# Performance work log

Hardware: AMD Instinct MI355X
Metric: run time of the kernel (lower is better)

Reference implementation:

```python
import jax, jax.numpy as jnp
import numpy as np


def _l2norm(x, eps=1e-12):
    # F.normalize(p=2, dim=-1): x / max(||x||_2, eps)
    n = jnp.linalg.norm(x, axis=-1, keepdims=True)
    return x / jnp.maximum(n, eps)


def _dwconv3x3(x, w):
    # depthwise 3x3 conv, padding=1, no bias. x: [B,C,H,W], w: [C,1,3,3]
    return jax.lax.conv_general_dilated(
        x, w, window_strides=(1, 1), padding='SAME',
        feature_group_count=x.shape[1],
        dimension_numbers=('NCHW', 'OIHW', 'NCHW'))


def setup_inputs() -> dict:
    key = jax.random.key(0)
    ks = jax.random.split(key, 10)
    B, H, W, C = 2, 256, 256, 64
    heads, dh, dim_out = 8, 64, 64
    hd = heads * dh  # 512
    s = 0.02
    return {
        'x_in': jax.random.normal(ks[0], (B, H, W, C), jnp.float32),
        'Wq': jax.random.normal(ks[1], (C, hd), jnp.float32) * s,
        'Wk': jax.random.normal(ks[2], (C, hd), jnp.float32) * s,
        'Wv': jax.random.normal(ks[3], (C, hd), jnp.float32) * s,
        'rescale': jnp.ones((heads, 1, 1), jnp.float32),
        'Wproj': jax.random.normal(ks[4], (hd, dim_out), jnp.float32) * s,
        'bproj': jnp.zeros((dim_out,), jnp.float32),
        'Wc1d': jax.random.normal(ks[5], (hd, dim_out), jnp.float32) * s,
        'bc1d': jnp.zeros((dim_out,), jnp.float32),
        'Wpe1': jax.random.normal(ks[6], (dim_out, 1, 3, 3), jnp.float32) * s,
        'Wpe2': jax.random.normal(ks[7], (dim_out, 1, 3, 3), jnp.float32) * s,
    }


def reference(x_in, Wq, Wk, Wv, rescale, Wproj, bproj, Wc1d, bc1d, Wpe1, Wpe2):
    b, h, w, c = x_in.shape
    heads = rescale.shape[0]
    hd = Wq.shape[1]
    dh = hd // heads
    dim_out = Wproj.shape[1]
    ds = 2

    # AvgPool2d(2,2) on channels-last input
    xp = x_in.reshape(b, h // ds, ds, w // ds, ds, c).mean(axis=(2, 4))
    n_ds = (h // ds) * (w // ds)
    xd = xp.reshape(b, n_ds, c)

    # q,k from downsampled tokens; v from full-res tokens
    q = (xd @ Wq).reshape(b, n_ds, heads, dh).transpose(0, 2, 3, 1)   # [b,heads,dh,n_ds]
    k = (xd @ Wk).reshape(b, n_ds, heads, dh).transpose(0, 2, 3, 1)   # [b,heads,dh,n_ds]
    v_inp = x_in.reshape(b, h * w, c) @ Wv                             # [b,n,hd]
    v = v_inp.reshape(b, h * w, heads, dh).transpose(0, 2, 3, 1)       # [b,heads,dh,n]

    q = _l2norm(q)
    k = _l2norm(k)

    # channel (transposed) attention: [b,heads,dh,dh]
    attn = jnp.einsum('bhin,bhjn->bhij', k, q) * rescale
    attn = jax.nn.softmax(attn, axis=-1)

    xa = jnp.einsum('bhij,bhjn->bhin', attn, v)                        # [b,heads,dh,n]
    xa = xa.transpose(0, 3, 1, 2).reshape(b, h * w, hd)                # [b,n,hd]
    out_c = (xa @ Wproj + bproj).reshape(b, h, w, dim_out)

    # positional branch: 1x1 conv (pointwise) then two depthwise 3x3 convs with GELU
    p = v_inp @ Wc1d + bc1d                                            # [b,n,dim_out]
    p = p.reshape(b, h, w, dim_out).transpose(0, 3, 1, 2)              # [b,dim_out,h,w]
    p = _dwconv3x3(p, Wpe1)
    p = jax.nn.gelu(p, approximate=False)
    p = _dwconv3x3(p, Wpe2)
    out_p = p.transpose(0, 2, 3, 1)                                    # [b,h,w,dim_out]

    return out_c + out_p
```

## Files before the change

kernel.cpp:

```cpp
#include <hip/hip_runtime.h>
#include <math.h>


typedef unsigned short u16;
typedef unsigned int u32;
typedef __attribute__((ext_vector_type(8))) short short8;
typedef __attribute__((ext_vector_type(4))) float f32x4;

__device__ __forceinline__ float bf2f(u16 h) { return __uint_as_float(((u32)h) << 16); }
__device__ __forceinline__ u16 f2bf(float f) {
    u32 u = __float_as_uint(f);
    return (u16)((u + 0x7fffu + ((u >> 16) & 1u)) >> 16);
}
__device__ __forceinline__ float rbf(float f) { return bf2f(f2bf(f)); }
__device__ __forceinline__ u32 pk2(float lo, float hi) {
    return (u32)f2bf(lo) | ((u32)f2bf(hi) << 16);
}
__device__ __forceinline__ void unpack8(uint4 v, float* f) {
    u32 a[4] = {v.x, v.y, v.z, v.w};
#pragma unroll
    for (int i = 0; i < 4; ++i) {
        f[2 * i]     = __uint_as_float(a[i] << 16);
        f[2 * i + 1] = __uint_as_float(a[i] & 0xffff0000u);
    }
}
__device__ __forceinline__ float gelu_exact(float v) {
    return 0.5f * v * (1.f + erff(v * 0.70710678118654752f));
}
__device__ __forceinline__ void splitbf(float g, short& hi, short& lo) {
    u16 hb = f2bf(g);
    hi = (short)hb;
    lo = (short)f2bf(g - bf2f(hb));
}

__global__ __launch_bounds__(256) void k_front(
    const float* __restrict__ x,
    const float* __restrict__ wq_f, const float* __restrict__ wk_f,
    const float* __restrict__ wv_f, const float* __restrict__ rs_f,
    const float* __restrict__ wp_f, const float* __restrict__ bp_f,
    const float* __restrict__ wc_f, const float* __restrict__ bc_f,
    const float* __restrict__ p1_f, const float* __restrict__ p2_f,
    u32* __restrict__ wb32, u16* __restrict__ wqT, u16* __restrict__ wkT,
    u16* __restrict__ wpT, float* __restrict__ Wpos,
    u16* __restrict__ xb, float* __restrict__ partials) {
    __shared__ float xvs[64 * 68];
    int blk = blockIdx.x;
    int t = threadIdx.x;
    if (blk < 323) {
        u32 pid = (u32)blk * 256u + t;
        if (pid < 82564u) {
            const float* src; u32 p;
            if      (pid < 16384u) { src = wq_f; p = pid; }
            else if (pid < 32768u) { src = wk_f; p = pid - 16384u; }
            else if (pid < 49152u) { src = wv_f; p = pid - 32768u; }
            else if (pid < 49156u) { src = rs_f; p = pid - 49152u; }
            else if (pid < 65540u) { src = wp_f; p = pid - 49156u; }
            else if (pid < 65572u) { src = bp_f; p = pid - 65540u; }
            else if (pid < 81956u) { src = wc_f; p = pid - 65572u; }
            else if (pid < 81988u) { src = bc_f; p = pid - 81956u; }
            else if (pid < 82276u) { src = p1_f; p = pid - 81988u; }
            else                   { src = p2_f; p = pid - 82276u; }
            wb32[pid] = (u32)f2bf(src[2 * p]) | ((u32)f2bf(src[2 * p + 1]) << 16);
            if (pid < 32768u) {
                u16* dstT = (pid < 16384u) ? wqT : wkT;
                u32 e0 = 2u * (pid & 16383u);
                u32 c = e0 >> 9, j = e0 & 511u;
                dstT[j * 64 + c]       = f2bf(src[e0]);
                dstT[(j + 1) * 64 + c] = f2bf(src[e0 + 1]);
            } else if (pid >= 49156u && pid < 65540u) {
                u32 e0 = 2u * (pid - 49156u);
                u32 ip = e0 >> 6, o = e0 & 63u;
                u32 base = (ip >> 6) * 4096u + (ip & 63u);
                wpT[base + o * 64]       = f2bf(src[e0]);
                wpT[base + (o + 1) * 64] = f2bf(src[e0 + 1]);
            }
        }
    } else if (blk < 387) {
        int c = blk - 323;
        int o = t & 63, ch = t >> 6;
        const float* wvr = wv_f + c * 512 + ch * 128;
        const float* wcr = wc_f + (size_t)(ch * 128) * 64 + o;
        float s = 0.f;
        for (int kk = 0; kk < 128; ++kk)
            s += rbf(wvr[kk]) * rbf(wcr[(size_t)kk * 64]);
        xvs[ch * 64 + o] = s;
        __syncthreads();
        if (t < 64)
            Wpos[c * 64 + t] = (xvs[t] + xvs[64 + t]) + (xvs[128 + t] + xvs[192 + t]);
    } else {
        int gb = blk - 387;
        int b = gb >> 8, sub = gb & 255;
        int py = sub >> 1, half = sub & 1;
        const size_t rowbase = (size_t)(b * 256 + 2 * py) * 16384 + (size_t)half * 8192;
#pragma unroll
        for (int i2 = 0; i2 < 4; ++i2) {
            int u = t + 256 * i2;
            int P = u >> 4, cq = u & 15;
            size_t o0 = rowbase + (size_t)(2 * P) * 64 + cq * 4;
            float4 a0 = *(const float4*)(x + o0);
            float4 a1 = *(const float4*)(x + o0 + 64);
            float4 a2 = *(const float4*)(x + o0 + 16384);
            float4 a3 = *(const float4*)(x + o0 + 16384 + 64);
            *(uint2*)(xb + o0)              = make_uint2(pk2(a0.x, a0.y), pk2(a0.z, a0.w));
            *(uint2*)(xb + o0 + 64)         = make_uint2(pk2(a1.x, a1.y), pk2(a1.z, a1.w));
            *(uint2*)(xb + o0 + 16384)      = make_uint2(pk2(a2.x, a2.y), pk2(a2.z, a2.w));
            *(uint2*)(xb + o0 + 16384 + 64) = make_uint2(pk2(a3.x, a3.y), pk2(a3.z, a3.w));
            float4 s;
            s.x = 0.25f * (a0.x + a1.x + a2.x + a3.x);
            s.y = 0.25f * (a0.y + a1.y + a2.y + a3.y);
            s.z = 0.25f * (a0.z + a1.z + a2.z + a3.z);
            s.w = 0.25f * (a0.w + a1.w + a2.w + a3.w);
            *(float4*)(&xvs[P * 68 + cq * 4]) = s;
        }
        __syncthreads();
        int r0 = (t >> 4) << 2, c0 = (t & 15) << 2;
        float acc[4][4] = {{0.f}};
        for (int P = 0; P < 64; ++P) {
            float4 av = *(const float4*)(&xvs[P * 68 + r0]);
            float4 bv = *(const float4*)(&xvs[P * 68 + c0]);
            float ar[4] = {av.x, av.y, av.z, av.w};
            float br[4] = {bv.x, bv.y, bv.z, bv.w};
#pragma unroll
            for (int i = 0; i < 4; ++i)
#pragma unroll
                for (int j = 0; j < 4; ++j)
                    acc[i][j] += ar[i] * br[j];
        }
        float* outp = partials + (size_t)gb * 4096;
#pragma unroll
        for (int i = 0; i < 4; ++i)
            *(float4*)(&outp[(r0 + i) * 64 + c0]) =
                make_float4(acc[i][0], acc[i][1], acc[i][2], acc[i][3]);
    }
}

__global__ __launch_bounds__(256) void k_mid1(
    const float* __restrict__ partials, float* __restrict__ G4, float* __restrict__ Weff,
    const u16* __restrict__ xb, const float* __restrict__ Wpos,
    const u16* __restrict__ bc1d, u16* __restrict__ pbuf) {
    __shared__ u16 sm[128 * 72];
    int blk = blockIdx.x;
    int t = threadIdx.x;
    if (blk < 128) {
        int gid = blk * 256 + t;
        int e = gid & 4095, ch = (gid >> 12) & 3, b = gid >> 14;
        const float* p0 = partials + ((size_t)(b * 256 + ch * 64)) * 4096 + e;
        float s = 0.f;
        for (int p = 0; p < 64; ++p)
            s += p0[(size_t)p * 4096];
        G4[gid] = s;
        if (gid < 8192) Weff[gid] = 0.f;
        return;
    }
    int pb = blk - 128;
    int lane = t & 63, wv = t >> 6;
    int col = lane & 15, quad = lane >> 4;

    short8 bf[2][4];
#pragma unroll
    for (int kh = 0; kh < 2; ++kh)
#pragma unroll
        for (int nt = 0; nt < 4; ++nt) {
            short8 v;
#pragma unroll
            for (int j = 0; j < 8; ++j)
                v[j] = (short)f2bf(Wpos[(kh * 32 + quad * 8 + j) * 64 + nt * 16 + col]);
            bf[kh][nt] = v;
        }
    float bias[4];
#pragma unroll
    for (int nt = 0; nt < 4; ++nt) bias[nt] = bf2f(bc1d[nt * 16 + col]);

    size_t base = (size_t)pb * 128;
#pragma unroll
    for (int g = 0; g < 2; ++g) {
        int P0 = wv * 32 + g * 16;
        const short8* ap = (const short8*)(xb + (base + P0 + col) * 64);
        short8 a0 = ap[quad];
        short8 a1 = ap[4 + quad];
#pragma unroll
        for (int nt = 0; nt < 4; ++nt) {
            f32x4 acc = {0.f, 0.f, 0.f, 0.f};
            acc = __builtin_amdgcn_mfma_f32_16x16x32_bf16(a0, bf[0][nt], acc, 0, 0, 0);
            acc = __builtin_amdgcn_mfma_f32_16x16x32_bf16(a1, bf[1][nt], acc, 0, 0, 0);
#pragma unroll
            for (int r = 0; r < 4; ++r)
                sm[(P0 + quad * 4 + r) * 72 + nt * 16 + col] = f2bf(acc[r] + bias[nt]);
        }
    }
    __syncthreads();
#pragma unroll
    for (int k = 0; k < 4; ++k) {
        int linear = k * 256 + t;
        int px = linear >> 3, oct = linear & 7;
        uint4 v = *(const uint4*)(&sm[px * 72 + oct * 8]);
        *(uint4*)(pbuf + (base + px) * 64 + oct * 8) = v;
    }
}

__global__ __launch_bounds__(256) void k_mid2(
    const u16* __restrict__ wqT, const u16* __restrict__ wkT,
    const u16* __restrict__ wpT, const u16* __restrict__ wvb,
    const u16* __restrict__ rsb,
    const float* __restrict__ G4, float* __restrict__ Weff,
    const u16* __restrict__ pbuf, const u16* __restrict__ wpe1, u16* __restrict__ tbuf) {
    __shared__ __align__(16) char shm[53248];
    int blk = blockIdx.x, t = threadIdx.x;
    if (blk < 16) {
        u16*   GhiL = (u16*)shm;
        u16*   GloL = (u16*)(shm + 9216);
        float* Lraw = (float*)shm;
        float* TkS  = (float*)(shm + 18432);
        float* TqS  = (float*)(shm + 35840);
        int b = blk >> 3, h = blk & 7;
        int lane = t & 63, w = t >> 6;
        int lr = lane & 15, lq = lane >> 4;
        {
            int base = t * 16;
            int row = base >> 6, col = base & 63;
            const float* Gb = G4 + (size_t)b * 16384;
#pragma unroll
            for (int half = 0; half < 2; ++half) {
                short8 hi8, lo8;
#pragma unroll
                for (int q = 0; q < 8; ++q) {
                    int e = base + half * 8 + q;
                    float g = (Gb[e] + Gb[4096 + e]) + (Gb[8192 + e] + Gb[12288 + e]);
                    short hh, ll; splitbf(g, hh, ll);
                    hi8[q] = hh; lo8[q] = ll;
                }
                *(short8*)(&GhiL[row * 72 + col + half * 8]) = hi8;
                *(short8*)(&GloL[row * 72 + col + half * 8]) = lo8;
            }
        }
        __syncthreads();
        {
            short8 ahi[2], alo[2];
#pragma unroll
            for (int ks = 0; ks < 2; ++ks) {
                ahi[ks] = *(const short8*)(&GhiL[(w * 16 + lr) * 72 + ks * 32 + lq * 8]);
                alo[ks] = *(const short8*)(&GloL[(w * 16 + lr) * 72 + ks * 32 + lq * 8]);
            }
#pragma unroll
            for (int sel = 0; sel < 2; ++sel) {
                const u16* WT = sel ? wqT : wkT;
                float* outp = sel ? TqS : TkS;
#pragma unroll
                for (int nt = 0; nt < 4; ++nt) {
                    f32x4 acc = {0.f, 0.f, 0.f, 0.f};
#pragma unroll
                    for (int ks = 0; ks < 2; ++ks) {
                        short8 bv = *(const short8*)(&WT[(h * 64 + nt * 16 + lr) * 64 + ks * 32 + lq * 8]);
                        acc = __builtin_amdgcn_mfma_f32_16x16x32_bf16(ahi[ks], bv, acc, 0, 0, 0);
                        acc = __builtin_amdgcn_mfma_f32_16x16x32_bf16(alo[ks], bv, acc, 0, 0, 0);
                    }
#pragma unroll
                    for (int r = 0; r < 4; ++r)
                        outp[(w * 16 + lq * 4 + r) * 68 + nt * 16 + lr] = acc[r];
                }
            }
        }
        __syncthreads();
        {
            int ci = t & 63, grp = t >> 6;
            const u16* wr = wkT + (h * 64 + ci) * 64 + grp * 16;
            float s = 0.f;
#pragma unroll
            for (int cc = 0; cc < 16; ++cc)
                s += bf2f(wr[cc]) * TkS[(grp * 16 + cc) * 68 + ci];
            TqS[ci * 68 + 64 + grp] = s;
        }
        __syncthreads();
        if (t < 64) {
            float s = (TqS[t * 68 + 64] + TqS[t * 68 + 65]) +
                      (TqS[t * 68 + 66] + TqS[t * 68 + 67]);
            TkS[t * 68 + 64] = fmaxf(sqrtf(fmaxf(s, 0.f)), 1e-12f);
        }
        {
            short8 ak[2];
#pragma unroll
            for (int ks = 0; ks < 2; ++ks)
                ak[ks] = *(const short8*)(&wkT[(h * 64 + w * 16 + lr) * 64 + ks * 32 + lq * 8]);
#pragma unroll
            for (int nt = 0; nt < 4; ++nt) {
                f32x4 acc = {0.f, 0.f, 0.f, 0.f};
#pragma unroll
                for (int ks = 0; ks < 2; ++ks) {
                    short8 bhi, blo;
#pragma unroll
                    for (int jj = 0; jj < 8; ++jj) {
                        short h16, l16;
                        splitbf(TqS[(ks * 32 + lq * 8 + jj) * 68 + nt * 16 + lr], h16, l16);
                        bhi[jj] = h16; blo[jj] = l16;
                    }
                    acc = __builtin_amdgcn_mfma_f32_16x16x32_bf16(ak[ks], bhi, acc, 0, 0, 0);
                    acc = __builtin_amdgcn_mfma_f32_16x16x32_bf16(ak[ks], blo, acc, 0, 0, 0);
                }
#pragma unroll
                for (int r = 0; r < 4; ++r)
                    Lraw[(w * 16 + lq * 4 + r) * 68 + nt * 16 + lr] = acc[r];
            }
        }
        __syncthreads();
        {
            int ci = t & 63, grp = t >> 6;
            const u16* wr = wqT + (h * 64 + ci) * 64 + grp * 16;
            float s = 0.f;
#pragma unroll
            for (int cc = 0; cc < 16; ++cc)
                s += bf2f(wr[cc]) * TqS[(grp * 16 + cc) * 68 + ci];
            TqS[ci * 68 + 64 + grp] = s;
        }
        __syncthreads();
        if (t < 64) {
            float s = (TqS[t * 68 + 64] + TqS[t * 68 + 65]) +
                      (TqS[t * 68 + 66] + TqS[t * 68 + 67]);
            TkS[t * 68 + 65] = fmaxf(sqrtf(fmaxf(s, 0.f)), 1e-12f);
        }
        __syncthreads();
        {
            int i = t >> 2, jq = t & 3, j0 = jq * 16;
            float L[16];
#pragma unroll
            for (int q = 0; q < 4; ++q) {
                float4 lv = *(const float4*)(&Lraw[i * 68 + j0 + 4 * q]);
                L[4 * q] = lv.x; L[4 * q + 1] = lv.y;
                L[4 * q + 2] = lv.z; L[4 * q + 3] = lv.w;
            }
            float rs = bf2f(rsb[h]);
            float nki = TkS[i * 68 + 64];
            float nqv[16];
#pragma unroll
            for (int jj = 0; jj < 16; ++jj) nqv[jj] = TkS[(j0 + jj) * 68 + 65];
            float m = -1e30f;
#pragma unroll
            for (int jj = 0; jj < 16; ++jj) {
                L[jj] = L[jj] * rs / (nki * nqv[jj]);
                m = fmaxf(m, L[jj]);
            }
            m = fmaxf(m, __shfl_xor(m, 1));
            m = fmaxf(m, __shfl_xor(m, 2));
            float s = 0.f;
#pragma unroll
            for (int jj = 0; jj < 16; ++jj) {
                L[jj] = __expf(L[jj] - m);
                s += L[jj];
            }
            s += __shfl_xor(s, 1);
            s += __shfl_xor(s, 2);
            float inv = 1.f / s;
#pragma unroll
            for (int q = 0; q < 4; ++q)
                *(float4*)(&Lraw[i * 68 + j0 + 4 * q]) =
                    make_float4(L[4 * q] * inv, L[4 * q + 1] * inv,
                                L[4 * q + 2] * inv, L[4 * q + 3] * inv);
        }
        __syncthreads();
        {
            short8 ahi[2], alo[2];
#pragma unroll
            for (int ks = 0; ks < 2; ++ks) {
                short8 hi, lo;
#pragma unroll
                for (int jj = 0; jj < 8; ++jj) {
                    short h16, l16;
                    splitbf(Lraw[(ks * 32 + lq * 8 + jj) * 68 + w * 16 + lr], h16, l16);
                    hi[jj] = h16; lo[jj] = l16;
                }
                ahi[ks] = hi; alo[ks] = lo;
            }
#pragma unroll
            for (int nt = 0; nt < 4; ++nt) {
                f32x4 acc = {0.f, 0.f, 0.f, 0.f};
#pragma unroll
                for (int ks = 0; ks < 2; ++ks) {
                    short8 bv = *(const short8*)(&wpT[h * 4096 + (nt * 16 + lr) * 64 + ks * 32 + lq * 8]);
                    acc = __builtin_amdgcn_mfma_f32_16x16x32_bf16(ahi[ks], bv, acc, 0, 0, 0);
                    acc = __builtin_amdgcn_mfma_f32_16x16x32_bf16(alo[ks], bv, acc, 0, 0, 0);
                }
#pragma unroll
                for (int r = 0; r < 4; ++r)
                    TkS[(w * 16 + lq * 4 + r) * 68 + nt * 16 + lr] = acc[r];
            }
        }
        __syncthreads();
        {
            short8 av[2];
#pragma unroll
            for (int ks = 0; ks < 2; ++ks)
                av[ks] = *(const short8*)(&wvb[(w * 16 + lr) * 512 + h * 64 + ks * 32 + lq * 8]);
            float* W = Weff + b * 4096;
#pragma unroll
            for (int nt = 0; nt < 4; ++nt) {
                f32x4 acc = {0.f, 0.f, 0.f, 0.f};
#pragma unroll
                for (int ks = 0; ks < 2; ++ks) {
                    short8 bhi, blo;
#pragma unroll
                    for (int jj = 0; jj < 8; ++jj) {
                        short h16, l16;
                        splitbf(TkS[(ks * 32 + lq * 8 + jj) * 68 + nt * 16 + lr], h16, l16);
                        bhi[jj] = h16; blo[jj] = l16;
                    }
                    acc = __builtin_amdgcn_mfma_f32_16x16x32_bf16(av[ks], bhi, acc, 0, 0, 0);
                    acc = __builtin_amdgcn_mfma_f32_16x16x32_bf16(av[ks], blo, acc, 0, 0, 0);
                }
#pragma unroll
                for (int r = 0; r < 4; ++r)
                    atomicAdd(&W[(w * 16 + lq * 4 + r) * 64 + nt * 16 + lr], acc[r]);
            }
        }
        return;
    }
    u16* sm = (u16*)shm;
    int cb = blk - 16;
    int b  = cb >> 9;
    int ty = (cb >> 3) & 63;
    int tx = cb & 7;
    int gy0 = ty * 4, gx0 = tx * 32;

    for (int i = t; i < 1632; i += 256) {
        int px = i >> 3, ch = i & 7;
        int hy = px / 34, hx = px - hy * 34;
        int gy = gy0 + hy - 1, gx = gx0 + hx - 1;
        uint4 v = make_uint4(0, 0, 0, 0);
        if ((unsigned)gy < 256u && (unsigned)gx < 256u)
            v = *(const uint4*)(pbuf + ((size_t)((b << 16) + (gy << 8) + gx)) * 64 + ch * 8);
        *(uint4*)(&sm[px * 72 + ch * 8]) = v;
    }
    int oct = t & 7;
    float w[8][9];
#pragma unroll
    for (int j = 0; j < 8; ++j)
#pragma unroll
        for (int k = 0; k < 9; ++k) w[j][k] = bf2f(wpe1[(oct * 8 + j) * 9 + k]);
    __syncthreads();

#pragma unroll
    for (int s = 0; s < 4; ++s) {
        int lp = (t >> 3) + s * 32;
        int ly = lp >> 5, lx = lp & 31;
        float acc[8] = {0.f, 0.f, 0.f, 0.f, 0.f, 0.f, 0.f, 0.f};
#pragma unroll
        for (int dy = 0; dy < 3; ++dy)
#pragma unroll
            for (int dx = 0; dx < 3; ++dx) {
                int hp = (ly + dy) * 34 + lx + dx;
                uint4 v = *(const uint4*)(&sm[hp * 72 + oct * 8]);
                float f[8];
                unpack8(v, f);
                int tap = dy * 3 + dx;
#pragma unroll
                for (int j = 0; j < 8; ++j) acc[j] += f[j] * w[j][tap];
            }
        u32 pk[4];
#pragma unroll
        for (int q = 0; q < 4; ++q)
            pk[q] = pk2(gelu_exact(acc[2 * q]), gelu_exact(acc[2 * q + 1]));
        size_t gpix = (size_t)(b << 16) + ((size_t)(gy0 + ly) << 8) + gx0 + lx;
        *(uint4*)(tbuf + gpix * 64 + oct * 8) = make_uint4(pk[0], pk[1], pk[2], pk[3]);
    }
}

__global__ __launch_bounds__(256) void k_final(const u16* __restrict__ xb,
                                               const u16* __restrict__ tbuf,
                                               const float* __restrict__ Weff,
                                               const u16* __restrict__ wpe2,
                                               const u16* __restrict__ bproj,
                                               float* __restrict__ out) {
    __shared__ u16 sm[204 * 72];
    __shared__ float stage[128 * 68];
    int t = threadIdx.x;
    int blk = blockIdx.x;
    int b  = blk >> 9;
    int ty = (blk >> 3) & 63;
    int tx = blk & 7;
    int gy0 = ty * 4, gx0 = tx * 32;

    for (int i = t; i < 1632; i += 256) {
        int px = i >> 3, ch = i & 7;
        int hy = px / 34, hx = px - hy * 34;
        int gy = gy0 + hy - 1, gx = gx0 + hx - 1;
        uint4 v = make_uint4(0, 0, 0, 0);
        if ((unsigned)gy < 256u && (unsigned)gx < 256u)
            v = *(const uint4*)(tbuf + ((size_t)((b << 16) + (gy << 8) + gx)) * 64 + ch * 8);
        *(uint4*)(&sm[px * 72 + ch * 8]) = v;
    }
    int oct = t & 7;
    {
        float w[8][9];
#pragma unroll
        for (int j = 0; j < 8; ++j)
#pragma unroll
            for (int k = 0; k < 9; ++k) w[j][k] = bf2f(wpe2[(oct * 8 + j) * 9 + k]);
        __syncthreads();
#pragma unroll
        for (int s = 0; s < 4; ++s) {
            int lp = (t >> 3) + s * 32;
            int ly = lp >> 5, lx = lp & 31;
            float acc[8] = {0.f, 0.f, 0.f, 0.f, 0.f, 0.f, 0.f, 0.f};
#pragma unroll
            for (int dy = 0; dy < 3; ++dy)
#pragma unroll
                for (int dx = 0; dx < 3; ++dx) {
                    int hp = (ly + dy) * 34 + lx + dx;
                    uint4 v = *(const uint4*)(&sm[hp * 72 + oct * 8]);
                    float f[8];
                    unpack8(v, f);
                    int tap = dy * 3 + dx;
#pragma unroll
                    for (int j = 0; j < 8; ++j) acc[j] += f[j] * w[j][tap];
                }
#pragma unroll
            for (int j = 0; j < 8; ++j)
                stage[lp * 68 + oct * 8 + j] = acc[j];
        }
    }
    __syncthreads();

    int lane = t & 63, wv = t >> 6;
    int col = lane & 15, quad = lane >> 4;
    const float* W = Weff + b * 4096;
    short8 bf[2][4];
#pragma unroll
    for (int kh = 0; kh < 2; ++kh)
#pragma unroll
        for (int nt = 0; nt < 4; ++nt) {
            short8 v;
#pragma unroll
            for (int j = 0; j < 8; ++j)
                v[j] = (short)f2bf(W[(kh * 32 + quad * 8 + j) * 64 + nt * 16 + col]);
            bf[kh][nt] = v;
        }
    float bias[4];
#pragma unroll
    for (int nt = 0; nt < 4; ++nt) bias[nt] = bf2f(bproj[nt * 16 + col]);

#pragma unroll
    for (int g = 0; g < 2; ++g) {
        int grp = wv * 2 + g;
        int ly = grp >> 1;
        int lxb = (grp & 1) * 16;
        size_t rowpix = (size_t)(b << 16) + ((size_t)(gy0 + ly) << 8) + gx0;
        const short8* ap = (const short8*)(xb + (rowpix + lxb + col) * 64);
        short8 a0 = ap[quad];
        short8 a1 = ap[4 + quad];
#pragma unroll
        for (int nt = 0; nt < 4; ++nt) {
            f32x4 acc = {0.f, 0.f, 0.f, 0.f};
            acc = __builtin_amdgcn_mfma_f32_16x16x32_bf16(a0, bf[0][nt], acc, 0, 0, 0);
            acc = __builtin_amdgcn_mfma_f32_16x16x32_bf16(a1, bf[1][nt], acc, 0, 0, 0);
#pragma unroll
            for (int r = 0; r < 4; ++r) {
                int lp = ly * 32 + lxb + quad * 4 + r;
                stage[lp * 68 + nt * 16 + col] += acc[r] + bias[nt];
            }
        }
    }
    __syncthreads();

#pragma unroll
    for (int k = 0; k < 8; ++k) {
        int linear = k * 256 + t;
        int px = linear >> 4, c4 = linear & 15;
        int ly = px >> 5, lx = px & 31;
        float4 v = *(const float4*)(&stage[px * 68 + c4 * 4]);
        size_t gpix = (size_t)(b << 16) + ((size_t)(gy0 + ly) << 8) + gx0 + lx;
        *(float4*)(out + gpix * 64 + c4 * 4) = v;
    }
}

extern "C" void kernel_launch(void* const* d_in, const int* in_sizes, int n_in,
                              void* d_out, int out_size, void* d_ws, size_t ws_size,
                              hipStream_t stream) {
    const float* x = (const float*)d_in[0];
    float* out = (float*)d_out;

    char* w = (char*)d_ws;
    size_t off = 0;
    auto alloc = [&](size_t bytes) -> void* {
        void* p = w + off;
        off += (bytes + 255) & ~(size_t)255;
        return p;
    };
    u16* xb = (u16*)alloc((size_t)16777216 * 2);
    u16* wb = (u16*)alloc((size_t)165128 * 2);
    u16* wqb = wb;
    u16* wkb = wqb + 32768;
    u16* wvb = wkb + 32768;
    u16* rsb = wvb + 32768;
    u16* wpb = rsb + 8;
    u16* bpb = wpb + 32768;
    u16* wcb = bpb + 64;
    u16* bcb = wcb + 32768;
    u16* p1b = bcb + 64;
    u16* p2b = p1b + 576;
    (void)wcb; (void)wqb; (void)wkb; (void)wpb;

    u16* wqT = (u16*)alloc((size_t)32768 * 2);
    u16* wkT = (u16*)alloc((size_t)32768 * 2);
    u16* wpT = (u16*)alloc((size_t)32768 * 2);

    float* partials = (float*)alloc((size_t)512 * 4096 * 4);
    float* G4       = (float*)alloc((size_t)2 * 4 * 4096 * 4);
    float* Weff     = (float*)alloc((size_t)2 * 4096 * 4);
    float* Wpos     = (float*)alloc((size_t)4096 * 4);
    u16*   pbuf     = (u16*)alloc((size_t)2 * 65536 * 64 * 2);
    u16*   tbuf     = (u16*)alloc((size_t)2 * 65536 * 64 * 2);

    hipLaunchKernelGGL(k_front, dim3(899), dim3(256), 0, stream,
                       x,
                       (const float*)d_in[1], (const float*)d_in[2], (const float*)d_in[3],
                       (const float*)d_in[4], (const float*)d_in[5], (const float*)d_in[6],
                       (const float*)d_in[7], (const float*)d_in[8], (const float*)d_in[9],
                       (const float*)d_in[10],
                       (u32*)wb, wqT, wkT, wpT, Wpos, xb, partials);
    hipLaunchKernelGGL(k_mid1, dim3(1152), dim3(256), 0, stream,
                       partials, G4, Weff, xb, Wpos, bcb, pbuf);
    hipLaunchKernelGGL(k_mid2, dim3(1040), dim3(256), 0, stream,
                       wqT, wkT, wpT, wvb, rsb, G4, Weff, pbuf, p1b, tbuf);
    hipLaunchKernelGGL(k_final, dim3(1024), dim3(256), 0, stream,
                       xb, tbuf, Weff, p2b, bpb, out);
}
```

Before: 155.1 us.

## Fuse Gram reduction via atomics and recompute pointwise conv inside dwconv tiles

```diff
diff --git a/kernel.cpp b/kernel.cpp
--- a/kernel.cpp
+++ b/kernel.cpp
@@ -42,7 +42,7 @@
     const float* __restrict__ p1_f, const float* __restrict__ p2_f,
     u32* __restrict__ wb32, u16* __restrict__ wqT, u16* __restrict__ wkT,
     u16* __restrict__ wpT, float* __restrict__ Wpos,
-    u16* __restrict__ xb, float* __restrict__ partials) {
+    u16* __restrict__ xb, float* __restrict__ G4) {
     __shared__ float xvs[64 * 68];
     int blk = blockIdx.x;
     int t = threadIdx.x;
@@ -126,75 +126,12 @@
                 for (int j = 0; j < 4; ++j)
                     acc[i][j] += ar[i] * br[j];
         }
-        float* outp = partials + (size_t)gb * 4096;
+        float* gout = G4 + ((size_t)(b * 4 + (sub & 3))) * 4096;
 #pragma unroll
         for (int i = 0; i < 4; ++i)
-            *(float4*)(&outp[(r0 + i) * 64 + c0]) =
-                make_float4(acc[i][0], acc[i][1], acc[i][2], acc[i][3]);
-    }
-}
-
-__global__ __launch_bounds__(256) void k_mid1(
-    const float* __restrict__ partials, float* __restrict__ G4, float* __restrict__ Weff,
-    const u16* __restrict__ xb, const float* __restrict__ Wpos,
-    const u16* __restrict__ bc1d, u16* __restrict__ pbuf) {
-    __shared__ u16 sm[128 * 72];
-    int blk = blockIdx.x;
-    int t = threadIdx.x;
-    if (blk < 128) {
-        int gid = blk * 256 + t;
-        int e = gid & 4095, ch = (gid >> 12) & 3, b = gid >> 14;
-        const float* p0 = partials + ((size_t)(b * 256 + ch * 64)) * 4096 + e;
-        float s = 0.f;
-        for (int p = 0; p < 64; ++p)
-            s += p0[(size_t)p * 4096];
-        G4[gid] = s;
-        if (gid < 8192) Weff[gid] = 0.f;
-        return;
-    }
-    int pb = blk - 128;
-    int lane = t & 63, wv = t >> 6;
-    int col = lane & 15, quad = lane >> 4;
-
-    short8 bf[2][4];
-#pragma unroll
-    for (int kh = 0; kh < 2; ++kh)
-#pragma unroll
-        for (int nt = 0; nt < 4; ++nt) {
-            short8 v;
-#pragma unroll
-            for (int j = 0; j < 8; ++j)
-                v[j] = (short)f2bf(Wpos[(kh * 32 + quad * 8 + j) * 64 + nt * 16 + col]);
-            bf[kh][nt] = v;
-        }
-    float bias[4];
-#pragma unroll
-    for (int nt = 0; nt < 4; ++nt) bias[nt] = bf2f(bc1d[nt * 16 + col]);
-
-    size_t base = (size_t)pb * 128;
-#pragma unroll
-    for (int g = 0; g < 2; ++g) {
-        int P0 = wv * 32 + g * 16;
-        const short8* ap = (const short8*)(xb + (base + P0 + col) * 64);
-        short8 a0 = ap[quad];
-        short8 a1 = ap[4 + quad];
-#pragma unroll
-        for (int nt = 0; nt < 4; ++nt) {
-            f32x4 acc = {0.f, 0.f, 0.f, 0.f};
-            acc = __builtin_amdgcn_mfma_f32_16x16x32_bf16(a0, bf[0][nt], acc, 0, 0, 0);
-            acc = __builtin_amdgcn_mfma_f32_16x16x32_bf16(a1, bf[1][nt], acc, 0, 0, 0);
-#pragma unroll
-            for (int r = 0; r < 4; ++r)
-                sm[(P0 + quad * 4 + r) * 72 + nt * 16 + col] = f2bf(acc[r] + bias[nt]);
-        }
-    }
-    __syncthreads();
-#pragma unroll
-    for (int k = 0; k < 4; ++k) {
-        int linear = k * 256 + t;
-        int px = linear >> 3, oct = linear & 7;
-        uint4 v = *(const uint4*)(&sm[px * 72 + oct * 8]);
-        *(uint4*)(pbuf + (base + px) * 64 + oct * 8) = v;
+#pragma unroll
+            for (int j = 0; j < 4; ++j)
+                atomicAdd(&gout[(r0 + i) * 64 + c0 + j], acc[i][j]);
     }
 }
 
@@ -203,7 +140,9 @@
     const u16* __restrict__ wpT, const u16* __restrict__ wvb,
     const u16* __restrict__ rsb,
     const float* __restrict__ G4, float* __restrict__ Weff,
-    const u16* __restrict__ pbuf, const u16* __restrict__ wpe1, u16* __restrict__ tbuf) {
+    const u16* __restrict__ xb, const float* __restrict__ Wpos,
+    const u16* __restrict__ bc1d, const u16* __restrict__ wpe1,
+    u16* __restrict__ tbuf) {
     __shared__ __align__(16) char shm[53248];
     int blk = blockIdx.x, t = threadIdx.x;
     if (blk < 16) {
@@ -418,15 +357,56 @@
     int ty = (cb >> 3) & 63;
     int tx = cb & 7;
     int gy0 = ty * 4, gx0 = tx * 32;
-
-    for (int i = t; i < 1632; i += 256) {
-        int px = i >> 3, ch = i & 7;
-        int hy = px / 34, hx = px - hy * 34;
-        int gy = gy0 + hy - 1, gx = gx0 + hx - 1;
-        uint4 v = make_uint4(0, 0, 0, 0);
-        if ((unsigned)gy < 256u && (unsigned)gx < 256u)
-            v = *(const uint4*)(pbuf + ((size_t)((b << 16) + (gy << 8) + gx)) * 64 + ch * 8);
-        *(uint4*)(&sm[px * 72 + ch * 8]) = v;
+    {
+        int lane = t & 63, wv = t >> 6;
+        int col = lane & 15, quad = lane >> 4;
+        short8 bfw[2][4];
+#pragma unroll
+        for (int kh = 0; kh < 2; ++kh)
+#pragma unroll
+            for (int nt = 0; nt < 4; ++nt) {
+                short8 v;
+#pragma unroll
+                for (int j = 0; j < 8; ++j)
+                    v[j] = (short)f2bf(Wpos[(kh * 32 + quad * 8 + j) * 64 + nt * 16 + col]);
+                bfw[kh][nt] = v;
+            }
+        float bias[4];
+#pragma unroll
+        for (int nt = 0; nt < 4; ++nt) bias[nt] = bf2f(bc1d[nt * 16 + col]);
+#pragma unroll
+        for (int g = 0; g < 4; ++g) {
+            int grp = wv * 4 + g;
+            int pa = grp * 16 + col;
+            int hya = pa / 34, hxa = pa - hya * 34;
+            int gya = gy0 + hya - 1, gxa = gx0 + hxa - 1;
+            bool ina = ((unsigned)gya < 256u) && ((unsigned)gxa < 256u) && (pa < 204);
+            size_t pix = ina ? ((size_t)(b << 16) + ((size_t)gya << 8) + gxa) : 0;
+            const short8* ap = (const short8*)(xb + pix * 64);
+            short8 a0 = ap[quad];
+            short8 a1 = ap[4 + quad];
+            f32x4 accs[4];
+#pragma unroll
+            for (int nt = 0; nt < 4; ++nt) {
+                f32x4 acc = {0.f, 0.f, 0.f, 0.f};
+                acc = __builtin_amdgcn_mfma_f32_16x16x32_bf16(a0, bfw[0][nt], acc, 0, 0, 0);
+                acc = __builtin_amdgcn_mfma_f32_16x16x32_bf16(a1, bfw[1][nt], acc, 0, 0, 0);
+                accs[nt] = acc;
+            }
+#pragma unroll
+            for (int r = 0; r < 4; ++r) {
+                int pc = grp * 16 + quad * 4 + r;
+                if (pc < 204) {
+                    int hyc = pc / 34, hxc = pc - hyc * 34;
+                    int gyc = gy0 + hyc - 1, gxc = gx0 + hxc - 1;
+                    bool inc = ((unsigned)gyc < 256u) && ((unsigned)gxc < 256u);
+#pragma unroll
+                    for (int nt = 0; nt < 4; ++nt)
+                        sm[pc * 72 + nt * 16 + col] =
+                            inc ? f2bf(accs[nt][r] + bias[nt]) : (u16)0;
+                }
+            }
+        }
     }
     int oct = t & 7;
     float w[8][9];
@@ -601,12 +581,13 @@
     u16* wkT = (u16*)alloc((size_t)32768 * 2);
     u16* wpT = (u16*)alloc((size_t)32768 * 2);
 
-    float* partials = (float*)alloc((size_t)512 * 4096 * 4);
-    float* G4       = (float*)alloc((size_t)2 * 4 * 4096 * 4);
-    float* Weff     = (float*)alloc((size_t)2 * 4096 * 4);
-    float* Wpos     = (float*)alloc((size_t)4096 * 4);
-    u16*   pbuf     = (u16*)alloc((size_t)2 * 65536 * 64 * 2);
-    u16*   tbuf     = (u16*)alloc((size_t)2 * 65536 * 64 * 2);
+    float* G4   = (float*)alloc((size_t)2 * 4 * 4096 * 4);
+    float* Weff = (float*)alloc((size_t)2 * 4096 * 4);
+    float* Wpos = (float*)alloc((size_t)4096 * 4);
+    u16*   tbuf = (u16*)alloc((size_t)2 * 65536 * 64 * 2);
+
+    hipMemsetAsync(G4, 0, (size_t)2 * 4 * 4096 * 4, stream);
+    hipMemsetAsync(Weff, 0, (size_t)2 * 4096 * 4, stream);
 
     hipLaunchKernelGGL(k_front, dim3(899), dim3(256), 0, stream,
                        x,
@@ -614,11 +595,9 @@
                        (const float*)d_in[4], (const float*)d_in[5], (const float*)d_in[6],
                        (const float*)d_in[7], (const float*)d_in[8], (const float*)d_in[9],
                        (const float*)d_in[10],
-                       (u32*)wb, wqT, wkT, wpT, Wpos, xb, partials);
-    hipLaunchKernelGGL(k_mid1, dim3(1152), dim3(256), 0, stream,
-                       partials, G4, Weff, xb, Wpos, bcb, pbuf);
+                       (u32*)wb, wqT, wkT, wpT, Wpos, xb, G4);
     hipLaunchKernelGGL(k_mid2, dim3(1040), dim3(256), 0, stream,
-                       wqT, wkT, wpT, wvb, rsb, G4, Weff, pbuf, p1b, tbuf);
+                       wqT, wkT, wpT, wvb, rsb, G4, Weff, xb, Wpos, bcb, p1b, tbuf);
     hipLaunchKernelGGL(k_final, dim3(1024), dim3(256), 0, stream,
                        xb, tbuf, Weff, p2b, bpb, out);
 }
```

New measurement: 183.7 us. 18.5% more time.

## Shrink LDS in mid2 and final kernels, pretranspose Wpos to bf16

Applied to the files above, without the earlier changes.

```diff
diff --git a/kernel.cpp b/kernel.cpp
--- a/kernel.cpp
+++ b/kernel.cpp
@@ -41,7 +41,7 @@
     const float* __restrict__ wc_f, const float* __restrict__ bc_f,
     const float* __restrict__ p1_f, const float* __restrict__ p2_f,
     u32* __restrict__ wb32, u16* __restrict__ wqT, u16* __restrict__ wkT,
-    u16* __restrict__ wpT, float* __restrict__ Wpos,
+    u16* __restrict__ wpT, float* __restrict__ Wpos, u16* __restrict__ wposT,
     u16* __restrict__ xb, float* __restrict__ partials) {
     __shared__ float xvs[64 * 68];
     int blk = blockIdx.x;
@@ -85,8 +85,11 @@
             s += rbf(wvr[kk]) * rbf(wcr[(size_t)kk * 64]);
         xvs[ch * 64 + o] = s;
         __syncthreads();
-        if (t < 64)
-            Wpos[c * 64 + t] = (xvs[t] + xvs[64 + t]) + (xvs[128 + t] + xvs[192 + t]);
+        if (t < 64) {
+            float v = (xvs[t] + xvs[64 + t]) + (xvs[128 + t] + xvs[192 + t]);
+            Wpos[c * 64 + t] = v;
+            wposT[t * 64 + c] = f2bf(v);
+        }
     } else {
         int gb = blk - 387;
         int b = gb >> 8, sub = gb & 255;
@@ -136,7 +139,7 @@
 
 __global__ __launch_bounds__(256) void k_mid1(
     const float* __restrict__ partials, float* __restrict__ G4, float* __restrict__ Weff,
-    const u16* __restrict__ xb, const float* __restrict__ Wpos,
+    const u16* __restrict__ xb, const u16* __restrict__ wposT,
     const u16* __restrict__ bc1d, u16* __restrict__ pbuf) {
     __shared__ u16 sm[128 * 72];
     int blk = blockIdx.x;
@@ -160,13 +163,8 @@
 #pragma unroll
     for (int kh = 0; kh < 2; ++kh)
 #pragma unroll
-        for (int nt = 0; nt < 4; ++nt) {
-            short8 v;
-#pragma unroll
-            for (int j = 0; j < 8; ++j)
-                v[j] = (short)f2bf(Wpos[(kh * 32 + quad * 8 + j) * 64 + nt * 16 + col]);
-            bf[kh][nt] = v;
-        }
+        for (int nt = 0; nt < 4; ++nt)
+            bf[kh][nt] = *(const short8*)(&wposT[(nt * 16 + col) * 64 + kh * 32 + quad * 8]);
     float bias[4];
 #pragma unroll
     for (int nt = 0; nt < 4; ++nt) bias[nt] = bf2f(bc1d[nt * 16 + col]);
@@ -203,15 +201,18 @@
     const u16* __restrict__ wpT, const u16* __restrict__ wvb,
     const u16* __restrict__ rsb,
     const float* __restrict__ G4, float* __restrict__ Weff,
-    const u16* __restrict__ pbuf, const u16* __restrict__ wpe1, u16* __restrict__ tbuf) {
-    __shared__ __align__(16) char shm[53248];
+    const u16* __restrict__ pbuf, const u16* __restrict__ wpe1,
+    u16* __restrict__ tbuf) {
+    __shared__ __align__(16) char shm[37376];
     int blk = blockIdx.x, t = threadIdx.x;
     if (blk < 16) {
         u16*   GhiL = (u16*)shm;
         u16*   GloL = (u16*)(shm + 9216);
-        float* Lraw = (float*)shm;
-        float* TkS  = (float*)(shm + 18432);
-        float* TqS  = (float*)(shm + 35840);
+        float* RG   = (float*)shm;
+        float* RA   = (float*)(shm + 18432);
+        float* scr  = (float*)(shm + 35840);
+        float* nkA  = (float*)(shm + 36864);
+        float* nqA  = (float*)(shm + 37120);
         int b = blk >> 3, h = blk & 7;
         int lane = t & 63, w = t >> 6;
         int lr = lane & 15, lq = lane >> 4;
@@ -234,30 +235,25 @@
             }
         }
         __syncthreads();
-        {
-            short8 ahi[2], alo[2];
-#pragma unroll
-            for (int ks = 0; ks < 2; ++ks) {
-                ahi[ks] = *(const short8*)(&GhiL[(w * 16 + lr) * 72 + ks * 32 + lq * 8]);
-                alo[ks] = *(const short8*)(&GloL[(w * 16 + lr) * 72 + ks * 32 + lq * 8]);
-            }
-#pragma unroll
-            for (int sel = 0; sel < 2; ++sel) {
-                const u16* WT = sel ? wqT : wkT;
-                float* outp = sel ? TqS : TkS;
-#pragma unroll
-                for (int nt = 0; nt < 4; ++nt) {
-                    f32x4 acc = {0.f, 0.f, 0.f, 0.f};
-#pragma unroll
-                    for (int ks = 0; ks < 2; ++ks) {
-                        short8 bv = *(const short8*)(&WT[(h * 64 + nt * 16 + lr) * 64 + ks * 32 + lq * 8]);
-                        acc = __builtin_amdgcn_mfma_f32_16x16x32_bf16(ahi[ks], bv, acc, 0, 0, 0);
-                        acc = __builtin_amdgcn_mfma_f32_16x16x32_bf16(alo[ks], bv, acc, 0, 0, 0);
-                    }
-#pragma unroll
-                    for (int r = 0; r < 4; ++r)
-                        outp[(w * 16 + lq * 4 + r) * 68 + nt * 16 + lr] = acc[r];
-                }
+        short8 ahi[2], alo[2];
+#pragma unroll
+        for (int ks = 0; ks < 2; ++ks) {
+            ahi[ks] = *(const short8*)(&GhiL[(w * 16 + lr) * 72 + ks * 32 + lq * 8]);
+            alo[ks] = *(const short8*)(&GloL[(w * 16 + lr) * 72 + ks * 32 + lq * 8]);
+        }
+        {
+#pragma unroll
+            for (int nt = 0; nt < 4; ++nt) {
+                f32x4 acc = {0.f, 0.f, 0.f, 0.f};
+#pragma unroll
+                for (int ks = 0; ks < 2; ++ks) {
+                    short8 bv = *(const short8*)(&wkT[(h * 64 + nt * 16 + lr) * 64 + ks * 32 + lq * 8]);
+                    acc = __builtin_amdgcn_mfma_f32_16x16x32_bf16(ahi[ks], bv, acc, 0, 0, 0);
+                    acc = __builtin_amdgcn_mfma_f32_16x16x32_bf16(alo[ks], bv, acc, 0, 0, 0);
+                }
+#pragma unroll
+                for (int r = 0; r < 4; ++r)
+                    RA[(w * 16 + lq * 4 + r) * 68 + nt * 16 + lr] = acc[r];
             }
         }
         __syncthreads();
@@ -267,16 +263,39 @@
             float s = 0.f;
 #pragma unroll
             for (int cc = 0; cc < 16; ++cc)
-                s += bf2f(wr[cc]) * TkS[(grp * 16 + cc) * 68 + ci];
-            TqS[ci * 68 + 64 + grp] = s;
+                s += bf2f(wr[cc]) * RA[(grp * 16 + cc) * 68 + ci];
+            scr[grp * 64 + ci] = s;
         }
         __syncthreads();
         if (t < 64) {
-            float s = (TqS[t * 68 + 64] + TqS[t * 68 + 65]) +
-                      (TqS[t * 68 + 66] + TqS[t * 68 + 67]);
-            TkS[t * 68 + 64] = fmaxf(sqrtf(fmaxf(s, 0.f)), 1e-12f);
-        }
-        {
+            float s = (scr[t] + scr[64 + t]) + (scr[128 + t] + scr[192 + t]);
+            nkA[t] = fmaxf(sqrtf(fmaxf(s, 0.f)), 1e-12f);
+        }
+        {
+#pragma unroll
+            for (int nt = 0; nt < 4; ++nt) {
+                f32x4 acc = {0.f, 0.f, 0.f, 0.f};
+#pragma unroll
+                for (int ks = 0; ks < 2; ++ks) {
+                    short8 bv = *(const short8*)(&wqT[(h * 64 + nt * 16 + lr) * 64 + ks * 32 + lq * 8]);
+                    acc = __builtin_amdgcn_mfma_f32_16x16x32_bf16(ahi[ks], bv, acc, 0, 0, 0);
+                    acc = __builtin_amdgcn_mfma_f32_16x16x32_bf16(alo[ks], bv, acc, 0, 0, 0);
+                }
+#pragma unroll
+                for (int r = 0; r < 4; ++r)
+                    RA[(w * 16 + lq * 4 + r) * 68 + nt * 16 + lr] = acc[r];
+            }
+        }
+        __syncthreads();
+        {
+            int ci = t & 63, grp = t >> 6;
+            const u16* wr = wqT + (h * 64 + ci) * 64 + grp * 16;
+            float s = 0.f;
+#pragma unroll
+            for (int cc = 0; cc < 16; ++cc)
+                s += bf2f(wr[cc]) * RA[(grp * 16 + cc) * 68 + ci];
+            scr[grp * 64 + ci] = s;
+
             short8 ak[2];
 #pragma unroll
             for (int ks = 0; ks < 2; ++ks)
@@ -290,7 +309,7 @@
 #pragma unroll
                     for (int jj = 0; jj < 8; ++jj) {
                         short h16, l16;
-                        splitbf(TqS[(ks * 32 + lq * 8 + jj) * 68 + nt * 16 + lr], h16, l16);
+                        splitbf(RA[(ks * 32 + lq * 8 + jj) * 68 + nt * 16 + lr], h16, l16);
                         bhi[jj] = h16; blo[jj] = l16;
                     }
                     acc = __builtin_amdgcn_mfma_f32_16x16x32_bf16(ak[ks], bhi, acc, 0, 0, 0);
@@ -298,24 +317,13 @@
                 }
 #pragma unroll
                 for (int r = 0; r < 4; ++r)
-                    Lraw[(w * 16 + lq * 4 + r) * 68 + nt * 16 + lr] = acc[r];
-            }
-        }
-        __syncthreads();
-        {
-            int ci = t & 63, grp = t >> 6;
-            const u16* wr = wqT + (h * 64 + ci) * 64 + grp * 16;
-            float s = 0.f;
-#pragma unroll
-            for (int cc = 0; cc < 16; ++cc)
-                s += bf2f(wr[cc]) * TqS[(grp * 16 + cc) * 68 + ci];
-            TqS[ci * 68 + 64 + grp] = s;
+                    RG[(w * 16 + lq * 4 + r) * 68 + nt * 16 + lr] = acc[r];
+            }
         }
         __syncthreads();
         if (t < 64) {
-            float s = (TqS[t * 68 + 64] + TqS[t * 68 + 65]) +
-                      (TqS[t * 68 + 66] + TqS[t * 68 + 67]);
-            TkS[t * 68 + 65] = fmaxf(sqrtf(fmaxf(s, 0.f)), 1e-12f);
+            float s = (scr[t] + scr[64 + t]) + (scr[128 + t] + scr[192 + t]);
+            nqA[t] = fmaxf(sqrtf(fmaxf(s, 0.f)), 1e-12f);
         }
         __syncthreads();
         {
@@ -323,15 +331,15 @@
             float L[16];
 #pragma unroll
             for (int q = 0; q < 4; ++q) {
-                float4 lv = *(const float4*)(&Lraw[i * 68 + j0 + 4 * q]);
+                float4 lv = *(const float4*)(&RG[i * 68 + j0 + 4 * q]);
                 L[4 * q] = lv.x; L[4 * q + 1] = lv.y;
                 L[4 * q + 2] = lv.z; L[4 * q + 3] = lv.w;
             }
             float rs = bf2f(rsb[h]);
-            float nki = TkS[i * 68 + 64];
+            float nki = nkA[i];
             float nqv[16];
 #pragma unroll
-            for (int jj = 0; jj < 16; ++jj) nqv[jj] = TkS[(j0 + jj) * 68 + 65];
+            for (int jj = 0; jj < 16; ++jj) nqv[jj] = nqA[j0 + jj];
             float m = -1e30f;
 #pragma unroll
             for (int jj = 0; jj < 16; ++jj) {
@@ -351,23 +359,23 @@
             float inv = 1.f / s;
 #pragma unroll
             for (int q = 0; q < 4; ++q)
-                *(float4*)(&Lraw[i * 68 + j0 + 4 * q]) =
+                *(float4*)(&RG[i * 68 + j0 + 4 * q]) =
                     make_float4(L[4 * q] * inv, L[4 * q + 1] * inv,
                                 L[4 * q + 2] * inv, L[4 * q + 3] * inv);
         }
         __syncthreads();
         {
-            short8 ahi[2], alo[2];
+            short8 phi[2], plo[2];
 #pragma unroll
             for (int ks = 0; ks < 2; ++ks) {
                 short8 hi, lo;
 #pragma unroll
                 for (int jj = 0; jj < 8; ++jj) {
                     short h16, l16;
-                    splitbf(Lraw[(ks * 32 + lq * 8 + jj) * 68 + w * 16 + lr], h16, l16);
+                    splitbf(RG[(ks * 32 + lq * 8 + jj) * 68 + w * 16 + lr], h16, l16);
                     hi[jj] = h16; lo[jj] = l16;
                 }
-                ahi[ks] = hi; alo[ks] = lo;
+                phi[ks] = hi; plo[ks] = lo;
             }
 #pragma unroll
             for (int nt = 0; nt < 4; ++nt) {
@@ -375,12 +383,12 @@
 #pragma unroll
                 for (int ks = 0; ks < 2; ++ks) {
                     short8 bv = *(const short8*)(&wpT[h * 4096 + (nt * 16 + lr) * 64 + ks * 32 + lq * 8]);
-                    acc = __builtin_amdgcn_mfma_f32_16x16x32_bf16(ahi[ks], bv, acc, 0, 0, 0);
-                    acc = __builtin_amdgcn_mfma_f32_16x16x32_bf16(alo[ks], bv, acc, 0, 0, 0);
+                    acc = __builtin_amdgcn_mfma_f32_16x16x32_bf16(phi[ks], bv, acc, 0, 0, 0);
+                    acc = __builtin_amdgcn_mfma_f32_16x16x32_bf16(plo[ks], bv, acc, 0, 0, 0);
                 }
 #pragma unroll
                 for (int r = 0; r < 4; ++r)
-                    TkS[(w * 16 + lq * 4 + r) * 68 + nt * 16 + lr] = acc[r];
+                    RA[(w * 16 + lq * 4 + r) * 68 + nt * 16 + lr] = acc[r];
             }
         }
         __syncthreads();
@@ -399,7 +407,7 @@
 #pragma unroll
                     for (int jj = 0; jj < 8; ++jj) {
                         short h16, l16;
-                        splitbf(TkS[(ks * 32 + lq * 8 + jj) * 68 + nt * 16 + lr], h16, l16);
+                        splitbf(RA[(ks * 32 + lq * 8 + jj) * 68 + nt * 16 + lr], h16, l16);
                         bhi[jj] = h16; blo[jj] = l16;
                     }
                     acc = __builtin_amdgcn_mfma_f32_16x16x32_bf16(av[ks], bhi, acc, 0, 0, 0);
@@ -468,8 +476,9 @@
                                                const u16* __restrict__ wpe2,
                                                const u16* __restrict__ bproj,
                                                float* __restrict__ out) {
-    __shared__ u16 sm[204 * 72];
-    __shared__ float stage[128 * 68];
+    __shared__ __align__(16) char shmf[34816];
+    u16*   sm    = (u16*)shmf;
+    float* stage = (float*)shmf;
     int t = threadIdx.x;
     int blk = blockIdx.x;
     int b  = blk >> 9;
@@ -487,6 +496,7 @@
         *(uint4*)(&sm[px * 72 + ch * 8]) = v;
     }
     int oct = t & 7;
+    u32 racc[4][4];
     {
         float w[8][9];
 #pragma unroll
@@ -512,8 +522,18 @@
                     for (int j = 0; j < 8; ++j) acc[j] += f[j] * w[j][tap];
                 }
 #pragma unroll
-            for (int j = 0; j < 8; ++j)
-                stage[lp * 68 + oct * 8 + j] = acc[j];
+            for (int q = 0; q < 4; ++q)
+                racc[s][q] = pk2(acc[2 * q], acc[2 * q + 1]);
+        }
+    }
+    __syncthreads();
+#pragma unroll
+    for (int s = 0; s < 4; ++s) {
+        int lp = (t >> 3) + s * 32;
+#pragma unroll
+        for (int q = 0; q < 4; ++q) {
+            stage[lp * 68 + oct * 8 + 2 * q]     = __uint_as_float(racc[s][q] << 16);
+            stage[lp * 68 + oct * 8 + 2 * q + 1] = __uint_as_float(racc[s][q] & 0xffff0000u);
         }
     }
     __syncthreads();
@@ -597,9 +617,10 @@
     u16* p2b = p1b + 576;
     (void)wcb; (void)wqb; (void)wkb; (void)wpb;
 
-    u16* wqT = (u16*)alloc((size_t)32768 * 2);
-    u16* wkT = (u16*)alloc((size_t)32768 * 2);
-    u16* wpT = (u16*)alloc((size_t)32768 * 2);
+    u16* wqT   = (u16*)alloc((size_t)32768 * 2);
+    u16* wkT   = (u16*)alloc((size_t)32768 * 2);
+    u16* wpT   = (u16*)alloc((size_t)32768 * 2);
+    u16* wposT = (u16*)alloc((size_t)4096 * 2);
 
     float* partials = (float*)alloc((size_t)512 * 4096 * 4);
     float* G4       = (float*)alloc((size_t)2 * 4 * 4096 * 4);
@@ -614,9 +635,9 @@
                        (const float*)d_in[4], (const float*)d_in[5], (const float*)d_in[6],
                        (const float*)d_in[7], (const float*)d_in[8], (const float*)d_in[9],
                        (const float*)d_in[10],
-                       (u32*)wb, wqT, wkT, wpT, Wpos, xb, partials);
+                       (u32*)wb, wqT, wkT, wpT, Wpos, wposT, xb, partials);
     hipLaunchKernelGGL(k_mid1, dim3(1152), dim3(256), 0, stream,
-                       partials, G4, Weff, xb, Wpos, bcb, pbuf);
+                       partials, G4, Weff, xb, wposT, bcb, pbuf);
     hipLaunchKernelGGL(k_mid2, dim3(1040), dim3(256), 0, stream,
                        wqT, wkT, wpT, wvb, rsb, G4, Weff, pbuf, p1b, tbuf);
     hipLaunchKernelGGL(k_final, dim3(1024), dim3(256), 0, stream,
```

Result: no change. 157.2 us (+1.4%).
